# Optimization experiments

Measured on AMD Instinct MI355X. Metric: run time of the kernel, lower is better.

The kernel has to match this reference:

```python
import jax, jax.numpy as jnp
import numpy as np

B, S, D, H = 4, 1024, 1024, 16
DEPTH = D // H


def setup_inputs() -> dict:
    key = jax.random.key(0)
    ks = jax.random.split(key, 12)
    scale = 1.0 / np.sqrt(D)
    return {
        "query": jax.random.normal(ks[0], (B, S, D), jnp.float32),
        "key_in": jax.random.normal(ks[1], (B, S, D), jnp.float32),
        "value": jax.random.normal(ks[2], (B, S, D), jnp.float32),
        "mask": jnp.zeros((B, 1, 1, S), jnp.float32),
        "wq": jax.random.normal(ks[3], (D, D), jnp.float32) * scale,
        "bq": jnp.zeros((D,), jnp.float32),
        "wk": jax.random.normal(ks[4], (D, D), jnp.float32) * scale,
        "bk": jnp.zeros((D,), jnp.float32),
        "wv": jax.random.normal(ks[5], (D, D), jnp.float32) * scale,
        "bv": jnp.zeros((D,), jnp.float32),
        "wo": jax.random.normal(ks[6], (D, D), jnp.float32) * scale,
        "bo": jnp.zeros((D,), jnp.float32),
    }


def _split_heads(x):
    b, s, _ = x.shape
    return x.reshape(b, s, H, DEPTH).transpose(0, 2, 1, 3)  # [B,H,S,depth]


def reference(query, key_in, value, mask, wq, bq, wk, bk, wv, bv, wo, bo):
    q = _split_heads(query @ wq + bq)
    k = _split_heads(key_in @ wk + bk)
    v = _split_heads(value @ wv + bv)
    # scaled dot-product attention, full O(S^2) scores as in the original
    scores = jnp.einsum("bhqd,bhkd->bhqk", q, k) / jnp.sqrt(jnp.float32(DEPTH))
    scores = scores + mask * (-1e9)
    attn = jax.nn.softmax(scores, axis=-1)
    ctx = jnp.einsum("bhqk,bhkd->bhqd", attn, v)
    concat = ctx.transpose(0, 2, 1, 3).reshape(query.shape[0], -1, D)
    return concat @ wo + bo
```

## Files before the change

### kernel.cpp

```cpp
#include <hip/hip_runtime.h>
#include <hip/hip_bf16.h>
#include <stdint.h>

#define B_ 4
#define S_ 1024
#define D_ 1024
#define H_ 16
#define DEPTH_ 64

typedef __attribute__((ext_vector_type(8))) short bf16x8;
typedef __attribute__((ext_vector_type(4))) float f32x4;
typedef unsigned short ubf16;

#define BAR() do { asm volatile("" ::: "memory"); __builtin_amdgcn_s_barrier(); asm volatile("" ::: "memory"); } while (0)

__device__ __forceinline__ ubf16 f2bf(float f) {
  union { float f; unsigned u; } v; v.f = f;
  unsigned r = v.u + 0x7fffu + ((v.u >> 16) & 1u);
  return (ubf16)(r >> 16);
}

__device__ __forceinline__ void async16(void* lds, const void* g) {
  __builtin_amdgcn_global_load_lds(
      (const __attribute__((address_space(1))) void*)g,
      (__attribute__((address_space(3))) void*)lds, 16, 0, 0);
}

struct Cvt3 { const float* src[3]; ubf16* dst[3]; };
__global__ __launch_bounds__(256) void convert3_bf16(Cvt3 a, int n4) {
  int i = blockIdx.x * 256 + threadIdx.x;
  const float* src = a.src[blockIdx.y];
  ubf16* dst = a.dst[blockIdx.y];
  if (i < n4) {
    float4 v = ((const float4*)src)[i];
    ushort4 o;
    o.x = f2bf(v.x); o.y = f2bf(v.y); o.z = f2bf(v.z); o.w = f2bf(v.w);
    ((ushort4*)dst)[i] = o;
  }
}

struct Tp4 { const float* W[4]; ubf16* WT[4]; };
__global__ __launch_bounds__(256) void transpose4_bf16(Tp4 a) {
  __shared__ float tile[32][33];
  const float* W = a.W[blockIdx.z];
  ubf16* WT = a.WT[blockIdx.z];
  int n0 = blockIdx.x * 32, k0 = blockIdx.y * 32;
  int tx = threadIdx.x & 31, ty = threadIdx.x >> 5;
#pragma unroll
  for (int i = 0; i < 4; ++i)
    tile[ty + i * 8][tx] = W[(size_t)(k0 + ty + i * 8) * D_ + n0 + tx];
  __syncthreads();
#pragma unroll
  for (int i = 0; i < 4; ++i)
    WT[(size_t)(n0 + ty + i * 8) * D_ + k0 + tx] = f2bf(tile[tx][ty + i * 8]);
}

struct GemmUnit {
  const ubf16* A; const ubf16* BT; const float* bias; void* out; int mode;
};
struct GemmArgs { GemmUnit u[3]; };

__global__ __launch_bounds__(256) void gemm_bt(GemmArgs args, int M, int N) {
  const GemmUnit gu = args.u[blockIdx.z];
  const int orig = blockIdx.x + (blockIdx.y << 3);
  const int xcd = orig & 7, j = orig >> 3;
  const int bm0 = (xcd * 4 + (j & 3)) * 128;
  const int bn0 = (j >> 2) * 128;
  const int tid = threadIdx.x, wid = tid >> 6, lane = tid & 63;
  const int wr = wid >> 1, wc = wid & 1;
  const int l15 = lane & 15, l4 = lane >> 4;
  const int K = 1024;

  __shared__ __align__(16) ubf16 As[3][128 * 32];
  __shared__ __align__(16) ubf16 Bs[3][128 * 32];
  f32x4 acc[4][4] = {};

  const ubf16* aCur[2]; const ubf16* bCur[2];
#pragma unroll
  for (int i = 0; i < 2; ++i) {
    int c = i * 256 + tid;
    int r = c >> 2, s = c & 3;
    int cg = s ^ ((r >> 1) & 3);
    aCur[i] = gu.A + (size_t)(bm0 + r) * K + cg * 8;
    bCur[i] = gu.BT + (size_t)(bn0 + r) * K + cg * 8;
  }
  auto stageAdv = [&](int bf) {
#pragma unroll
    for (int i = 0; i < 2; ++i) {
      async16((char*)&As[bf][0] + i * 4096 + wid * 1024, aCur[i]);
      async16((char*)&Bs[bf][0] + i * 4096 + wid * 1024, bCur[i]);
      aCur[i] += 32; bCur[i] += 32;
    }
  };
  int aOff[4], bOff[4];
#pragma unroll
  for (int f = 0; f < 4; ++f) {
    int ra = wr * 64 + f * 16 + l15;
    aOff[f] = ra * 64 + (l4 ^ ((ra >> 1) & 3)) * 16;
    int rb = wc * 64 + f * 16 + l15;
    bOff[f] = rb * 64 + (l4 ^ ((rb >> 1) & 3)) * 16;
  }
  auto body = [&](int bf) {
    bf16x8 af[4], bfr[4];
#pragma unroll
    for (int mi = 0; mi < 4; ++mi)
      af[mi] = *(const bf16x8*)((const char*)&As[bf][0] + aOff[mi]);
#pragma unroll
    for (int ni = 0; ni < 4; ++ni)
      bfr[ni] = *(const bf16x8*)((const char*)&Bs[bf][0] + bOff[ni]);
#pragma unroll
    for (int mi = 0; mi < 4; ++mi)
#pragma unroll
      for (int ni = 0; ni < 4; ++ni)
        acc[mi][ni] = __builtin_amdgcn_mfma_f32_16x16x32_bf16(af[mi], bfr[ni], acc[mi][ni], 0, 0, 0);
  };

  stageAdv(0); stageAdv(1);
#pragma unroll 1
  for (int tt = 0; tt < 10; ++tt) {
#pragma unroll
    for (int u = 0; u < 3; ++u) {
      stageAdv((u + 2) % 3);
      asm volatile("s_waitcnt vmcnt(8)" ::: "memory");
      BAR();
      body(u);
      BAR();
    }
  }
  asm volatile("s_waitcnt vmcnt(4)" ::: "memory");
  BAR();
  body(0);
  BAR();
  asm volatile("s_waitcnt vmcnt(0)" ::: "memory");
  BAR();
  body(1);

  float bv[4];
#pragma unroll
  for (int ni = 0; ni < 4; ++ni) bv[ni] = gu.bias[bn0 + wc * 64 + ni * 16 + l15];
#pragma unroll
  for (int mi = 0; mi < 4; ++mi) {
#pragma unroll
    for (int ni = 0; ni < 4; ++ni) {
#pragma unroll
      for (int r = 0; r < 4; ++r) {
        int m = bm0 + wr * 64 + mi * 16 + l4 * 4 + r;
        int n = bn0 + wc * 64 + ni * 16 + l15;
        float v = acc[mi][ni][r] + bv[ni];
        if (gu.mode == 0) {
          ((ubf16*)gu.out)[(size_t)m * N + n] = f2bf(v);
        } else if (gu.mode == 1) {
          int b = m >> 10, s = m & 1023, h = n >> 6, d = n & 63;
          ((ubf16*)gu.out)[(((size_t)(b * H_ + h)) * DEPTH_ + d) * S_ + s] = f2bf(v);
        } else {
          ((float*)gu.out)[(size_t)m * N + n] = v;
        }
      }
    }
  }
}

__global__ __launch_bounds__(256) void attention_fwd(
    const ubf16* __restrict__ Q, const ubf16* __restrict__ Kg,
    const ubf16* __restrict__ VT, const float* __restrict__ mask,
    ubf16* __restrict__ ctx) {
  const int lid = blockIdx.y * 8 + blockIdx.x;
  const int t0 = (lid & 7) * 64 + (lid >> 3);
  const int qt = t0 & 7, bh = t0 >> 3;
  const int b = bh >> 4, h = bh & 15;
  const int tid = threadIdx.x, wid = tid >> 6, lane = tid & 63;
  const int l15 = lane & 15, l4 = lane >> 4;
  const int q0 = qt * 128 + wid * 32;

  __shared__ __align__(16) ubf16 Ks[2][4096];
  __shared__ __align__(16) ubf16 Vs[2][4096];
  __shared__ __align__(16) ubf16 Ps[4][32][72];

  const ubf16* kb = Kg + ((size_t)(b * S_)) * D_ + h * DEPTH_;
  const ubf16* vb = VT + ((size_t)bh) * DEPTH_ * S_;

  bf16x8 aq[2][2];
#pragma unroll
  for (int mi = 0; mi < 2; ++mi)
#pragma unroll
    for (int kk = 0; kk < 2; ++kk)
      aq[mi][kk] = *(const bf16x8*)&Q[((size_t)(b * S_ + q0 + mi * 16 + l15)) * D_ +
                                      h * DEPTH_ + kk * 32 + l4 * 8];

  bf16x8 ones;
#pragma unroll
  for (int j = 0; j < 8; ++j) ones[j] = (short)0x3F80;

  f32x4 cacc[2][4] = {};
  f32x4 csum[2] = {};

  const float* mrow = mask + b * S_;
  const float C1 = 0.125f * 1.44269504f;
  const float CM = -1.0e9f * 1.44269504f;

  auto stage = [&](int bf, int kt) {
#pragma unroll
    for (int i = 0; i < 2; ++i) {
      int c = i * 256 + tid;
      int r = c >> 3, cg = (c & 7) ^ (r & 7);
      async16((char*)&Ks[bf][0] + i * 4096 + wid * 1024,
              kb + (size_t)(kt + r) * D_ + cg * 8);
      async16((char*)&Vs[bf][0] + i * 4096 + wid * 1024,
              vb + (size_t)r * S_ + kt + cg * 8);
    }
  };

  stage(0, 0);
  __syncthreads();

  for (int t = 0; t < 16; ++t) {
    const int cur = t & 1;
    const int kt = t * 64;
    if (t < 15) stage(cur ^ 1, kt + 64);

    bf16x8 kf[4][2];
#pragma unroll
    for (int nf = 0; nf < 4; ++nf)
#pragma unroll
      for (int kk = 0; kk < 2; ++kk) {
        int kr = nf * 16 + l15;
        int c16 = (kk * 4 + l4) ^ (kr & 7);
        kf[nf][kk] = *(const bf16x8*)((const char*)&Ks[cur][0] + kr * 128 + c16 * 16);
      }
    bf16x8 vf[4][2];
#pragma unroll
    for (int df = 0; df < 4; ++df)
#pragma unroll
      for (int kk = 0; kk < 2; ++kk) {
        int dr = df * 16 + l15;
        int c16 = (kk * 4 + l4) ^ (dr & 7);
        vf[df][kk] = *(const bf16x8*)((const char*)&Vs[cur][0] + dr * 128 + c16 * 16);
      }

    f32x4 sc[2][4];
#pragma unroll
    for (int mi = 0; mi < 2; ++mi)
#pragma unroll
      for (int nf = 0; nf < 4; ++nf) {
        f32x4 z = {0.f, 0.f, 0.f, 0.f};
        z = __builtin_amdgcn_mfma_f32_16x16x32_bf16(aq[mi][0], kf[nf][0], z, 0, 0, 0);
        z = __builtin_amdgcn_mfma_f32_16x16x32_bf16(aq[mi][1], kf[nf][1], z, 0, 0, 0);
        sc[mi][nf] = z;
      }

    float mvl[4];
#pragma unroll
    for (int nf = 0; nf < 4; ++nf) mvl[nf] = mrow[kt + nf * 16 + l15] * CM;

#pragma unroll
    for (int mi = 0; mi < 2; ++mi)
#pragma unroll
      for (int nf = 0; nf < 4; ++nf)
#pragma unroll
        for (int r = 0; r < 4; ++r) {
          float p = __builtin_amdgcn_exp2f(fmaf(sc[mi][nf][r], C1, mvl[nf]));
          Ps[wid][mi * 16 + l4 * 4 + r][nf * 16 + l15] = f2bf(p);
        }

    bf16x8 pf[2][2];
#pragma unroll
    for (int mi = 0; mi < 2; ++mi)
#pragma unroll
      for (int kk = 0; kk < 2; ++kk)
        pf[mi][kk] = *(const bf16x8*)&Ps[wid][mi * 16 + l15][kk * 32 + l4 * 8];

#pragma unroll
    for (int mi = 0; mi < 2; ++mi) {
#pragma unroll
      for (int df = 0; df < 4; ++df) {
        cacc[mi][df] = __builtin_amdgcn_mfma_f32_16x16x32_bf16(pf[mi][0], vf[df][0], cacc[mi][df], 0, 0, 0);
        cacc[mi][df] = __builtin_amdgcn_mfma_f32_16x16x32_bf16(pf[mi][1], vf[df][1], cacc[mi][df], 0, 0, 0);
      }
      csum[mi] = __builtin_amdgcn_mfma_f32_16x16x32_bf16(pf[mi][0], ones, csum[mi], 0, 0, 0);
      csum[mi] = __builtin_amdgcn_mfma_f32_16x16x32_bf16(pf[mi][1], ones, csum[mi], 0, 0, 0);
    }

    __syncthreads();
  }

#pragma unroll
  for (int mi = 0; mi < 2; ++mi) {
    float inv[4];
#pragma unroll
    for (int r = 0; r < 4; ++r) inv[r] = 1.0f / csum[mi][r];
#pragma unroll
    for (int df = 0; df < 4; ++df)
#pragma unroll
      for (int r = 0; r < 4; ++r) {
        int srow = q0 + mi * 16 + l4 * 4 + r;
        float v = cacc[mi][df][r] * inv[r];
        ctx[((size_t)(b * S_ + srow)) * D_ + h * DEPTH_ + df * 16 + l15] = f2bf(v);
      }
  }
}

extern "C" void kernel_launch(void* const* d_in, const int* in_sizes, int n_in,
                              void* d_out, int out_size, void* d_ws, size_t ws_size,
                              hipStream_t stream) {
  const float* query  = (const float*)d_in[0];
  const float* key_in = (const float*)d_in[1];
  const float* value  = (const float*)d_in[2];
  const float* mask   = (const float*)d_in[3];
  const float* wq = (const float*)d_in[4];
  const float* bq = (const float*)d_in[5];
  const float* wk = (const float*)d_in[6];
  const float* bk = (const float*)d_in[7];
  const float* wv = (const float*)d_in[8];
  const float* bv = (const float*)d_in[9];
  const float* wo = (const float*)d_in[10];
  const float* bo = (const float*)d_in[11];

  char* ws = (char*)d_ws;
  const size_t MB = 1024 * 1024;
  ubf16* Xq  = (ubf16*)(ws + 0 * MB);
  ubf16* Xk  = (ubf16*)(ws + 8 * MB);
  ubf16* Xv  = (ubf16*)(ws + 16 * MB);
  ubf16* WqT = (ubf16*)(ws + 24 * MB);
  ubf16* WkT = (ubf16*)(ws + 26 * MB);
  ubf16* WvT = (ubf16*)(ws + 28 * MB);
  ubf16* WoT = (ubf16*)(ws + 30 * MB);
  ubf16* Qb  = (ubf16*)(ws + 32 * MB);
  ubf16* Kb  = (ubf16*)(ws + 40 * MB);
  ubf16* VTb = (ubf16*)(ws + 48 * MB);
  ubf16* Ctx = (ubf16*)(ws + 56 * MB);

  const int n4 = (B_ * S_ * D_) / 4;
  Cvt3 c3;
  c3.src[0] = query;  c3.dst[0] = Xq;
  c3.src[1] = key_in; c3.dst[1] = Xk;
  c3.src[2] = value;  c3.dst[2] = Xv;
  convert3_bf16<<<dim3((n4 + 255) / 256, 3), dim3(256), 0, stream>>>(c3, n4);

  Tp4 t4;
  t4.W[0] = wq; t4.WT[0] = WqT;
  t4.W[1] = wk; t4.WT[1] = WkT;
  t4.W[2] = wv; t4.WT[2] = WvT;
  t4.W[3] = wo; t4.WT[3] = WoT;
  transpose4_bf16<<<dim3(32, 32, 4), dim3(256), 0, stream>>>(t4);

  GemmArgs g1;
  g1.u[0] = {Xq, WqT, bq, (void*)Qb, 0};
  g1.u[1] = {Xk, WkT, bk, (void*)Kb, 0};
  g1.u[2] = {Xv, WvT, bv, (void*)VTb, 1};
  gemm_bt<<<dim3(8, 32, 3), dim3(256), 0, stream>>>(g1, 4096, 1024);

  attention_fwd<<<dim3(8, 64), dim3(256), 0, stream>>>(Qb, Kb, VTb, mask, Ctx);

  GemmArgs g2;
  g2.u[0] = {Ctx, WoT, bo, d_out, 2};
  g2.u[1] = g2.u[0];
  g2.u[2] = g2.u[0];
  gemm_bt<<<dim3(8, 32, 1), dim3(256), 0, stream>>>(g2, 4096, 1024);
}
```

Baseline: 128.9 us.

## Fuse fp32-to-bf16 input conversion into QKV projection GEMM

Removes the separate conversion kernel for query/key/value. The QKV GEMM now loads fp32 activations directly through registers, converts them to bf16 and writes them into LDS, while the weights still use async global-to-LDS loads. This avoids writing and re-reading 24MB of bf16 intermediates and one kernel launch. The cost is double the global read bytes for A per tile and register-staged loads that cannot use the async LDS path. The output-projection GEMM also drops from triple to double buffering with a simpler loop, which may reduce latency hiding.

```diff
diff --git a/kernel.cpp b/kernel.cpp
--- a/kernel.cpp
+++ b/kernel.cpp
@@ -24,19 +24,6 @@
   __builtin_amdgcn_global_load_lds(
       (const __attribute__((address_space(1))) void*)g,
       (__attribute__((address_space(3))) void*)lds, 16, 0, 0);
-}
-
-struct Cvt3 { const float* src[3]; ubf16* dst[3]; };
-__global__ __launch_bounds__(256) void convert3_bf16(Cvt3 a, int n4) {
-  int i = blockIdx.x * 256 + threadIdx.x;
-  const float* src = a.src[blockIdx.y];
-  ubf16* dst = a.dst[blockIdx.y];
-  if (i < n4) {
-    float4 v = ((const float4*)src)[i];
-    ushort4 o;
-    o.x = f2bf(v.x); o.y = f2bf(v.y); o.z = f2bf(v.z); o.w = f2bf(v.w);
-    ((ushort4*)dst)[i] = o;
-  }
 }
 
 struct Tp4 { const float* W[4]; ubf16* WT[4]; };
@@ -53,6 +40,133 @@
 #pragma unroll
   for (int i = 0; i < 4; ++i)
     WT[(size_t)(n0 + ty + i * 8) * D_ + k0 + tx] = f2bf(tile[tx][ty + i * 8]);
+}
+
+struct GemmUnitF {
+  const float* A; const ubf16* BT; const float* bias; void* out; int mode;
+};
+struct GemmArgsF { GemmUnitF u[3]; };
+
+__global__ __launch_bounds__(256) void gemm_qkv_fused(GemmArgsF args) {
+  const GemmUnitF gu = args.u[blockIdx.z];
+  const int orig = blockIdx.x + (blockIdx.y << 3);
+  const int xcd = orig & 7, j = orig >> 3;
+  const int bm0 = (xcd * 4 + (j & 3)) * 128;
+  const int bn0 = (j >> 2) * 128;
+  const int tid = threadIdx.x, wid = tid >> 6, lane = tid & 63;
+  const int wr = wid >> 1, wc = wid & 1;
+  const int l15 = lane & 15, l4 = lane >> 4;
+  const int K = 1024;
+
+  __shared__ __align__(16) ubf16 As[2][128 * 32];
+  __shared__ __align__(16) ubf16 Bs[2][128 * 32];
+  f32x4 acc[4][4] = {};
+
+  int cc0, cc1;
+  const float* aP0; const float* aP1;
+  const ubf16* bP0; const ubf16* bP1;
+  {
+    cc0 = tid;           int r0 = cc0 >> 2, s0 = cc0 & 3, g0 = s0 ^ ((r0 >> 1) & 3);
+    cc1 = 256 + tid;     int r1 = cc1 >> 2, s1 = cc1 & 3, g1 = s1 ^ ((r1 >> 1) & 3);
+    aP0 = gu.A + (size_t)(bm0 + r0) * K + g0 * 8;
+    aP1 = gu.A + (size_t)(bm0 + r1) * K + g1 * 8;
+    bP0 = gu.BT + (size_t)(bn0 + r0) * K + g0 * 8;
+    bP1 = gu.BT + (size_t)(bn0 + r1) * K + g1 * 8;
+  }
+  int aOff[4], bOff[4];
+#pragma unroll
+  for (int f = 0; f < 4; ++f) {
+    int ra = wr * 64 + f * 16 + l15;
+    aOff[f] = ra * 64 + (l4 ^ ((ra >> 1) & 3)) * 16;
+    int rb = wc * 64 + f * 16 + l15;
+    bOff[f] = rb * 64 + (l4 ^ ((rb >> 1) & 3)) * 16;
+  }
+
+  {
+    async16((char*)&Bs[0][0] + wid * 1024, bP0); bP0 += 32;
+    async16((char*)&Bs[0][0] + 4096 + wid * 1024, bP1); bP1 += 32;
+    f32x4 a00 = *(const f32x4*)aP0, a01 = *(const f32x4*)(aP0 + 4); aP0 += 32;
+    f32x4 a10 = *(const f32x4*)aP1, a11 = *(const f32x4*)(aP1 + 4); aP1 += 32;
+    bf16x8 w0, w1;
+#pragma unroll
+    for (int q = 0; q < 4; ++q) {
+      w0[q] = (short)f2bf(a00[q]); w0[4 + q] = (short)f2bf(a01[q]);
+      w1[q] = (short)f2bf(a10[q]); w1[4 + q] = (short)f2bf(a11[q]);
+    }
+    *(bf16x8*)((char*)&As[0][0] + cc0 * 16) = w0;
+    *(bf16x8*)((char*)&As[0][0] + cc1 * 16) = w1;
+    asm volatile("s_waitcnt vmcnt(0) lgkmcnt(0)" ::: "memory");
+  }
+  BAR();
+
+#pragma unroll 1
+  for (int t = 0; t < 31; ++t) {
+    const int cur = t & 1;
+    async16((char*)&Bs[cur ^ 1][0] + wid * 1024, bP0); bP0 += 32;
+    async16((char*)&Bs[cur ^ 1][0] + 4096 + wid * 1024, bP1); bP1 += 32;
+    f32x4 a00 = *(const f32x4*)aP0, a01 = *(const f32x4*)(aP0 + 4); aP0 += 32;
+    f32x4 a10 = *(const f32x4*)aP1, a11 = *(const f32x4*)(aP1 + 4); aP1 += 32;
+    __builtin_amdgcn_sched_barrier(0);
+    bf16x8 af[4], bfr[4];
+#pragma unroll
+    for (int mi = 0; mi < 4; ++mi)
+      af[mi] = *(const bf16x8*)((const char*)&As[cur][0] + aOff[mi]);
+#pragma unroll
+    for (int ni = 0; ni < 4; ++ni)
+      bfr[ni] = *(const bf16x8*)((const char*)&Bs[cur][0] + bOff[ni]);
+#pragma unroll
+    for (int mi = 0; mi < 4; ++mi)
+#pragma unroll
+      for (int ni = 0; ni < 4; ++ni)
+        acc[mi][ni] = __builtin_amdgcn_mfma_f32_16x16x32_bf16(af[mi], bfr[ni], acc[mi][ni], 0, 0, 0);
+    __builtin_amdgcn_sched_barrier(0);
+    bf16x8 w0, w1;
+#pragma unroll
+    for (int q = 0; q < 4; ++q) {
+      w0[q] = (short)f2bf(a00[q]); w0[4 + q] = (short)f2bf(a01[q]);
+      w1[q] = (short)f2bf(a10[q]); w1[4 + q] = (short)f2bf(a11[q]);
+    }
+    *(bf16x8*)((char*)&As[cur ^ 1][0] + cc0 * 16) = w0;
+    *(bf16x8*)((char*)&As[cur ^ 1][0] + cc1 * 16) = w1;
+    asm volatile("s_waitcnt vmcnt(0) lgkmcnt(0)" ::: "memory");
+    BAR();
+  }
+  {
+    bf16x8 af[4], bfr[4];
+#pragma unroll
+    for (int mi = 0; mi < 4; ++mi)
+      af[mi] = *(const bf16x8*)((const char*)&As[1][0] + aOff[mi]);
+#pragma unroll
+    for (int ni = 0; ni < 4; ++ni)
+      bfr[ni] = *(const bf16x8*)((const char*)&Bs[1][0] + bOff[ni]);
+#pragma unroll
+    for (int mi = 0; mi < 4; ++mi)
+#pragma unroll
+      for (int ni = 0; ni < 4; ++ni)
+        acc[mi][ni] = __builtin_amdgcn_mfma_f32_16x16x32_bf16(af[mi], bfr[ni], acc[mi][ni], 0, 0, 0);
+  }
+
+  float bv[4];
+#pragma unroll
+  for (int ni = 0; ni < 4; ++ni) bv[ni] = gu.bias[bn0 + wc * 64 + ni * 16 + l15];
+#pragma unroll
+  for (int mi = 0; mi < 4; ++mi) {
+#pragma unroll
+    for (int ni = 0; ni < 4; ++ni) {
+#pragma unroll
+      for (int r = 0; r < 4; ++r) {
+        int m = bm0 + wr * 64 + mi * 16 + l4 * 4 + r;
+        int n = bn0 + wc * 64 + ni * 16 + l15;
+        float v = acc[mi][ni][r] + bv[ni];
+        if (gu.mode == 0) {
+          ((ubf16*)gu.out)[(size_t)m * 1024 + n] = f2bf(v);
+        } else {
+          int b = m >> 10, s = m & 1023, h = n >> 6, d = n & 63;
+          ((ubf16*)gu.out)[(((size_t)(b * H_ + h)) * DEPTH_ + d) * S_ + s] = f2bf(v);
+        }
+      }
+    }
+  }
 }
 
 struct GemmUnit {
@@ -71,8 +185,8 @@
   const int l15 = lane & 15, l4 = lane >> 4;
   const int K = 1024;
 
-  __shared__ __align__(16) ubf16 As[3][128 * 32];
-  __shared__ __align__(16) ubf16 Bs[3][128 * 32];
+  __shared__ __align__(16) ubf16 As[2][128 * 32];
+  __shared__ __align__(16) ubf16 Bs[2][128 * 32];
   f32x4 acc[4][4] = {};
 
   const ubf16* aCur[2]; const ubf16* bCur[2];
@@ -100,40 +214,31 @@
     int rb = wc * 64 + f * 16 + l15;
     bOff[f] = rb * 64 + (l4 ^ ((rb >> 1) & 3)) * 16;
   }
-  auto body = [&](int bf) {
+
+  stageAdv(0);
+  for (int t = 0; t < 32; ++t) {
+    const int cur = t & 1;
+    if (t < 31) {
+      stageAdv(cur ^ 1);
+      asm volatile("s_waitcnt vmcnt(4)" ::: "memory");
+    } else {
+      asm volatile("s_waitcnt vmcnt(0)" ::: "memory");
+    }
+    BAR();
     bf16x8 af[4], bfr[4];
 #pragma unroll
     for (int mi = 0; mi < 4; ++mi)
-      af[mi] = *(const bf16x8*)((const char*)&As[bf][0] + aOff[mi]);
+      af[mi] = *(const bf16x8*)((const char*)&As[cur][0] + aOff[mi]);
 #pragma unroll
     for (int ni = 0; ni < 4; ++ni)
-      bfr[ni] = *(const bf16x8*)((const char*)&Bs[bf][0] + bOff[ni]);
+      bfr[ni] = *(const bf16x8*)((const char*)&Bs[cur][0] + bOff[ni]);
 #pragma unroll
     for (int mi = 0; mi < 4; ++mi)
 #pragma unroll
       for (int ni = 0; ni < 4; ++ni)
         acc[mi][ni] = __builtin_amdgcn_mfma_f32_16x16x32_bf16(af[mi], bfr[ni], acc[mi][ni], 0, 0, 0);
-  };
-
-  stageAdv(0); stageAdv(1);
-#pragma unroll 1
-  for (int tt = 0; tt < 10; ++tt) {
-#pragma unroll
-    for (int u = 0; u < 3; ++u) {
-      stageAdv((u + 2) % 3);
-      asm volatile("s_waitcnt vmcnt(8)" ::: "memory");
-      BAR();
-      body(u);
-      BAR();
-    }
-  }
-  asm volatile("s_waitcnt vmcnt(4)" ::: "memory");
-  BAR();
-  body(0);
-  BAR();
-  asm volatile("s_waitcnt vmcnt(0)" ::: "memory");
-  BAR();
-  body(1);
+    BAR();
+  }
 
   float bv[4];
 #pragma unroll
@@ -317,9 +422,6 @@
 
   char* ws = (char*)d_ws;
   const size_t MB = 1024 * 1024;
-  ubf16* Xq  = (ubf16*)(ws + 0 * MB);
-  ubf16* Xk  = (ubf16*)(ws + 8 * MB);
-  ubf16* Xv  = (ubf16*)(ws + 16 * MB);
   ubf16* WqT = (ubf16*)(ws + 24 * MB);
   ubf16* WkT = (ubf16*)(ws + 26 * MB);
   ubf16* WvT = (ubf16*)(ws + 28 * MB);
@@ -329,13 +431,6 @@
   ubf16* VTb = (ubf16*)(ws + 48 * MB);
   ubf16* Ctx = (ubf16*)(ws + 56 * MB);
 
-  const int n4 = (B_ * S_ * D_) / 4;
-  Cvt3 c3;
-  c3.src[0] = query;  c3.dst[0] = Xq;
-  c3.src[1] = key_in; c3.dst[1] = Xk;
-  c3.src[2] = value;  c3.dst[2] = Xv;
-  convert3_bf16<<<dim3((n4 + 255) / 256, 3), dim3(256), 0, stream>>>(c3, n4);
-
   Tp4 t4;
   t4.W[0] = wq; t4.WT[0] = WqT;
   t4.W[1] = wk; t4.WT[1] = WkT;
@@ -343,11 +438,11 @@
   t4.W[3] = wo; t4.WT[3] = WoT;
   transpose4_bf16<<<dim3(32, 32, 4), dim3(256), 0, stream>>>(t4);
 
-  GemmArgs g1;
-  g1.u[0] = {Xq, WqT, bq, (void*)Qb, 0};
-  g1.u[1] = {Xk, WkT, bk, (void*)Kb, 0};
-  g1.u[2] = {Xv, WvT, bv, (void*)VTb, 1};
-  gemm_bt<<<dim3(8, 32, 3), dim3(256), 0, stream>>>(g1, 4096, 1024);
+  GemmArgsF g1;
+  g1.u[0] = {query,  WqT, bq, (void*)Qb, 0};
+  g1.u[1] = {key_in, WkT, bk, (void*)Kb, 0};
+  g1.u[2] = {value,  WvT, bv, (void*)VTb, 1};
+  gemm_qkv_fused<<<dim3(8, 32, 3), dim3(256), 0, stream>>>(g1);
 
   attention_fwd<<<dim3(8, 64), dim3(256), 0, stream>>>(Qb, Kb, VTb, mask, Ctx);
 
```

Result: faster. 126.2 us (-2.1%).

## Add 256x256 8-wave QKV GEMM with split A/B staging, simplify gemm_bt to double buffer

Applied to the files above, without the earlier changes.

The QKV projection moves to a new kernel with 256x256 tiles, 512 threads and 192 workgroups remapped across XCDs. It splits each K-step into two MFMA halves with interleaved A/B async staging, raises wave priority around the MFMA blocks, and keeps a triple buffer. The aim is more data reuse per tile and better overlap of loads with math. The output GEMM's gemm_bt is changed from a triple-buffered unrolled pipeline to a simpler double-buffered loop, which may expose more load latency there.

```diff
diff --git a/kernel.cpp b/kernel.cpp
--- a/kernel.cpp
+++ b/kernel.cpp
@@ -60,6 +60,132 @@
 };
 struct GemmArgs { GemmUnit u[3]; };
 
+__global__ __launch_bounds__(512) void gemm_qkv8(GemmArgs args) {
+  const int lin = blockIdx.x;
+  const int wg = (lin & 7) * 24 + (lin >> 3);
+  const int z = wg >> 6, rr = wg & 63;
+  const GemmUnit gu = args.u[z];
+  const int bm0 = (rr >> 2) * 256, bn0 = (rr & 3) * 256;
+  const int tid = threadIdx.x, wid = tid >> 6, lane = tid & 63;
+  const int wm = wid >> 2, wn = wid & 3;
+  const int l15 = lane & 15, l4 = lane >> 4;
+  const int K = 1024;
+
+  __shared__ __align__(16) ubf16 As[3][256 * 32];
+  __shared__ __align__(16) ubf16 Bs[3][256 * 32];
+  f32x4 acc[8][4] = {};
+
+  const ubf16* aP[2]; const ubf16* bP[2];
+#pragma unroll
+  for (int i = 0; i < 2; ++i) {
+    int c = i * 512 + tid;
+    int r = c >> 2, s = c & 3;
+    int cg = s ^ ((r >> 1) & 3);
+    aP[i] = gu.A + (size_t)(bm0 + r) * K + cg * 8;
+    bP[i] = gu.BT + (size_t)(bn0 + r) * K + cg * 8;
+  }
+  auto stageA = [&](int bf) {
+#pragma unroll
+    for (int i = 0; i < 2; ++i) {
+      async16((char*)&As[bf][0] + i * 8192 + wid * 1024, aP[i]);
+      aP[i] += 32;
+    }
+  };
+  auto stageB = [&](int bf) {
+#pragma unroll
+    for (int i = 0; i < 2; ++i) {
+      async16((char*)&Bs[bf][0] + i * 8192 + wid * 1024, bP[i]);
+      bP[i] += 32;
+    }
+  };
+  int aOff[8], bOff[4];
+#pragma unroll
+  for (int f = 0; f < 8; ++f) {
+    int ra = wm * 128 + f * 16 + l15;
+    aOff[f] = ra * 64 + (l4 ^ ((ra >> 1) & 3)) * 16;
+  }
+#pragma unroll
+  for (int f = 0; f < 4; ++f) {
+    int rb = wn * 64 + f * 16 + l15;
+    bOff[f] = rb * 64 + (l4 ^ ((rb >> 1) & 3)) * 16;
+  }
+
+  stageA(0); stageB(0);
+  stageA(1); stageB(1);
+  asm volatile("s_waitcnt vmcnt(4)" ::: "memory");
+  BAR();
+
+  int cur = 0, stg = 2;
+#pragma unroll 1
+  for (int t = 0; t < 32; ++t) {
+    const char* Ac = (const char*)&As[cur][0];
+    const char* Bc = (const char*)&Bs[cur][0];
+    bf16x8 af0[4], bfr[4];
+#pragma unroll
+    for (int mi = 0; mi < 4; ++mi)
+      af0[mi] = *(const bf16x8*)(Ac + aOff[mi]);
+#pragma unroll
+    for (int ni = 0; ni < 4; ++ni)
+      bfr[ni] = *(const bf16x8*)(Bc + bOff[ni]);
+    if (t < 30) stageA(stg);
+    __builtin_amdgcn_s_barrier();
+    asm volatile("s_waitcnt lgkmcnt(0)" ::: "memory");
+    __builtin_amdgcn_sched_barrier(0);
+    __builtin_amdgcn_s_setprio(1);
+#pragma unroll
+    for (int mi = 0; mi < 4; ++mi)
+#pragma unroll
+      for (int ni = 0; ni < 4; ++ni)
+        acc[mi][ni] = __builtin_amdgcn_mfma_f32_16x16x32_bf16(af0[mi], bfr[ni], acc[mi][ni], 0, 0, 0);
+    __builtin_amdgcn_s_setprio(0);
+    asm volatile("" ::: "memory");
+    __builtin_amdgcn_s_barrier();
+    asm volatile("" ::: "memory");
+    bf16x8 af1[4];
+#pragma unroll
+    for (int mi = 0; mi < 4; ++mi)
+      af1[mi] = *(const bf16x8*)(Ac + aOff[4 + mi]);
+    if (t < 30) stageB(stg);
+    __builtin_amdgcn_s_barrier();
+    asm volatile("s_waitcnt lgkmcnt(0)" ::: "memory");
+    __builtin_amdgcn_sched_barrier(0);
+    __builtin_amdgcn_s_setprio(1);
+#pragma unroll
+    for (int mi = 0; mi < 4; ++mi)
+#pragma unroll
+      for (int ni = 0; ni < 4; ++ni)
+        acc[4 + mi][ni] = __builtin_amdgcn_mfma_f32_16x16x32_bf16(af1[mi], bfr[ni], acc[4 + mi][ni], 0, 0, 0);
+    __builtin_amdgcn_s_setprio(0);
+    if (t < 30)       asm volatile("s_waitcnt vmcnt(4)" ::: "memory");
+    else if (t == 30) asm volatile("s_waitcnt vmcnt(0)" ::: "memory");
+    asm volatile("" ::: "memory");
+    __builtin_amdgcn_s_barrier();
+    asm volatile("" ::: "memory");
+    cur = (cur == 2) ? 0 : cur + 1;
+    stg = (stg == 2) ? 0 : stg + 1;
+  }
+
+  float bv[4];
+#pragma unroll
+  for (int ni = 0; ni < 4; ++ni) bv[ni] = gu.bias[bn0 + wn * 64 + ni * 16 + l15];
+#pragma unroll
+  for (int mi = 0; mi < 8; ++mi)
+#pragma unroll
+    for (int ni = 0; ni < 4; ++ni)
+#pragma unroll
+      for (int r = 0; r < 4; ++r) {
+        int m = bm0 + wm * 128 + mi * 16 + l4 * 4 + r;
+        int n = bn0 + wn * 64 + ni * 16 + l15;
+        float v = acc[mi][ni][r] + bv[ni];
+        if (gu.mode == 0) {
+          ((ubf16*)gu.out)[(size_t)m * 1024 + n] = f2bf(v);
+        } else {
+          int b = m >> 10, s = m & 1023, h = n >> 6, d = n & 63;
+          ((ubf16*)gu.out)[(((size_t)(b * H_ + h)) * DEPTH_ + d) * S_ + s] = f2bf(v);
+        }
+      }
+}
+
 __global__ __launch_bounds__(256) void gemm_bt(GemmArgs args, int M, int N) {
   const GemmUnit gu = args.u[blockIdx.z];
   const int orig = blockIdx.x + (blockIdx.y << 3);
@@ -71,8 +197,8 @@
   const int l15 = lane & 15, l4 = lane >> 4;
   const int K = 1024;
 
-  __shared__ __align__(16) ubf16 As[3][128 * 32];
-  __shared__ __align__(16) ubf16 Bs[3][128 * 32];
+  __shared__ __align__(16) ubf16 As[2][128 * 32];
+  __shared__ __align__(16) ubf16 Bs[2][128 * 32];
   f32x4 acc[4][4] = {};
 
   const ubf16* aCur[2]; const ubf16* bCur[2];
@@ -100,40 +226,31 @@
     int rb = wc * 64 + f * 16 + l15;
     bOff[f] = rb * 64 + (l4 ^ ((rb >> 1) & 3)) * 16;
   }
-  auto body = [&](int bf) {
+
+  stageAdv(0);
+  for (int t = 0; t < 32; ++t) {
+    const int cur = t & 1;
+    if (t < 31) {
+      stageAdv(cur ^ 1);
+      asm volatile("s_waitcnt vmcnt(4)" ::: "memory");
+    } else {
+      asm volatile("s_waitcnt vmcnt(0)" ::: "memory");
+    }
+    BAR();
     bf16x8 af[4], bfr[4];
 #pragma unroll
     for (int mi = 0; mi < 4; ++mi)
-      af[mi] = *(const bf16x8*)((const char*)&As[bf][0] + aOff[mi]);
+      af[mi] = *(const bf16x8*)((const char*)&As[cur][0] + aOff[mi]);
 #pragma unroll
     for (int ni = 0; ni < 4; ++ni)
-      bfr[ni] = *(const bf16x8*)((const char*)&Bs[bf][0] + bOff[ni]);
+      bfr[ni] = *(const bf16x8*)((const char*)&Bs[cur][0] + bOff[ni]);
 #pragma unroll
     for (int mi = 0; mi < 4; ++mi)
 #pragma unroll
       for (int ni = 0; ni < 4; ++ni)
         acc[mi][ni] = __builtin_amdgcn_mfma_f32_16x16x32_bf16(af[mi], bfr[ni], acc[mi][ni], 0, 0, 0);
-  };
-
-  stageAdv(0); stageAdv(1);
-#pragma unroll 1
-  for (int tt = 0; tt < 10; ++tt) {
-#pragma unroll
-    for (int u = 0; u < 3; ++u) {
-      stageAdv((u + 2) % 3);
-      asm volatile("s_waitcnt vmcnt(8)" ::: "memory");
-      BAR();
-      body(u);
-      BAR();
-    }
-  }
-  asm volatile("s_waitcnt vmcnt(4)" ::: "memory");
-  BAR();
-  body(0);
-  BAR();
-  asm volatile("s_waitcnt vmcnt(0)" ::: "memory");
-  BAR();
-  body(1);
+    BAR();
+  }
 
   float bv[4];
 #pragma unroll
@@ -347,7 +464,7 @@
   g1.u[0] = {Xq, WqT, bq, (void*)Qb, 0};
   g1.u[1] = {Xk, WkT, bk, (void*)Kb, 0};
   g1.u[2] = {Xv, WvT, bv, (void*)VTb, 1};
-  gemm_bt<<<dim3(8, 32, 3), dim3(256), 0, stream>>>(g1, 4096, 1024);
+  gemm_qkv8<<<dim3(192), dim3(512), 0, stream>>>(g1);
 
   attention_fwd<<<dim3(8, 64), dim3(256), 0, stream>>>(Qb, Kb, VTb, mask, Ctx);
 
```

Result: slower. 148.4 us (+15.1%).
